# Performance work log

Measured on AMD Instinct MI355X. Metric: run time of the kernel, lower is better.

Reference implementation:

```python
import jax, jax.numpy as jnp
import numpy as np

MU, LMBD = 1000.0, 5000.0
C1, C2 = 0.5, 0.5
SPACING = 1.0
EPS = 1e-8

# Cyclic minor indices: the 2x2 minor of entry (m,i) of a 3x3 matrix uses rows
# (m+1, m+2) mod 3 and cols (i+1, i+2) mod 3; det of that minor IS the signed
# cofactor (so minorSigns3d == ones, matching the original module's contract).
_r = (np.arange(3)[:, None, None, None] + 1 + np.arange(2)[None, None, :, None]) % 3
_c = (np.arange(3)[None, :, None, None] + 1 + np.arange(2)[None, None, None, :]) % 3
ROW_IDX = np.broadcast_to(_r, (3, 3, 2, 2))  # (m,i,p,q) -> row index into 3x3
COL_IDX = np.broadcast_to(_c, (3, 3, 2, 2))  # (m,i,p,q) -> col index into 3x3


def _cof2(M):
    # signed cofactor matrix of 2x2 matrices; M: (..., 2, 2)
    a, b = M[..., 0, 0], M[..., 0, 1]
    c, d = M[..., 1, 0], M[..., 1, 1]
    return jnp.stack([jnp.stack([d, -c], -1), jnp.stack([-b, a], -1)], -2)


def _div_pk1_neohook(gradU, hessU, mu, lmbd):
    # gradU: (b,i,j,k,3,3)  [d2=component, d1=spatial deriv]
    # hessU: (b,i,j,k,3,3,3) [d2, d1, d3]
    F = gradU + jnp.eye(3, dtype=gradU.dtype)
    idxF = F[..., ROW_IDX, COL_IDX]                                   # (...,3,3,2,2)
    cofF = idxF[..., 0, 0] * idxF[..., 1, 1] - idxF[..., 0, 1] * idxF[..., 1, 0]  # (...,3,3)
    idxHess = hessU[..., ROW_IDX, COL_IDX, :]                          # (...,3,3,2,2,3)
    # d/dx_j det(minor(F)[m,i]) = cof2(minor) : d(minor)/dx_j
    gradCofF = jnp.einsum('...mipq,...mipqj->...mij', _cof2(idxF), idxHess)
    F0, cofF0 = F[..., :, 0], cofF[..., :, 0]
    J = jnp.einsum('...m,...m->...', F0, cofF0) + EPS                  # det(F), col-0 expansion
    invJ = 1.0 / J
    gradJ = jnp.einsum('...m,...mj->...j', cofF0, hessU[..., :, 0, :]) \
          + jnp.einsum('...mj,...m->...j', gradCofF[..., :, 0, :], F0)
    divInvF_T = -jnp.einsum('...,...j,...mj->...m', invJ * invJ, gradJ, cofF) \
              + invJ[..., None] * jnp.einsum('...mjj->...m', gradCofF)
    divF = jnp.einsum('...mjj->...m', hessU)
    divPK1 = mu * (divF - divInvF_T)
    divPK1 = divPK1 + 0.5 * lmbd * (J * J - 1.0)[..., None] * divInvF_T
    divPK1 = divPK1 + lmbd * jnp.einsum('...ij,...j->...i', cofF, gradJ)
    return divPK1


def _phy_loss(pred):
    # pred: (b,i,j,k,3); central differences interior, one-sided at edges
    gradU = jnp.stack(jnp.gradient(pred, axis=(1, 2, 3)), axis=-1) / SPACING   # (b,i,j,k,3,3)
    hessU = jnp.stack(jnp.gradient(gradU, axis=(1, 2, 3)), axis=-1) / SPACING  # (b,i,j,k,3,3,3)
    r = _div_pk1_neohook(gradU, hessU, MU, LMBD)
    r = jnp.where(jnp.isnan(r), 0.0, r)  # r[r != r] = 0
    return jnp.mean(jnp.linalg.norm(r, axis=-1))


def setup_inputs() -> dict:
    key = jax.random.key(0)
    k1, k2 = jax.random.split(key)
    shape = (4, 64, 64, 64, 3)
    prediction = 0.01 * jax.random.normal(k1, shape, dtype=jnp.float32)
    target = 0.01 * jax.random.normal(k2, shape, dtype=jnp.float32)
    return {"prediction": prediction, "target": target}


def reference(prediction, target):
    mse_loss = jnp.mean((prediction - target) ** 2)
    phy_loss = _phy_loss(prediction)
    return C1 * mse_loss + C2 * phy_loss
```

## Files before the change

kernel.cpp:

```cpp
#include <hip/hip_runtime.h>
#include <math.h>

#define ND 64
#define NPTS (4 * ND * ND * ND)
#define SXG (ND * ND * 3)
#define SYG (ND * 3)
#define XSEG 4

struct f3 { float v[3]; };

__device__ __forceinline__ f3 comb2(float a, const f3& X, float s, const f3& Y) {
    f3 r;
#pragma unroll
    for (int c = 0; c < 3; c++) r.v[c] = a * X.v[c] + s * Y.v[c];
    return r;
}
__device__ __forceinline__ f3 comb3(float a, const f3& X, float s, const f3& Y, float u, const f3& Z) {
    f3 r;
#pragma unroll
    for (int c = 0; c < 3; c++) r.v[c] = a * X.v[c] + s * Y.v[c] + u * Z.v[c];
    return r;
}

__device__ __forceinline__ float phys_norm(const float F[3][3], const float H[3][6]) {
    constexpr int SYM[3][3] = {{0, 3, 4}, {3, 1, 5}, {4, 5, 2}};

    float cof[3][3];
#pragma unroll
    for (int i = 0; i < 3; i++) {
        const int i1 = (i + 1) % 3, i2 = (i + 2) % 3;
#pragma unroll
        for (int j = 0; j < 3; j++) {
            const int j1 = (j + 1) % 3, j2 = (j + 2) % 3;
            cof[i][j] = F[i1][j1] * F[i2][j2] - F[i1][j2] * F[i2][j1];
        }
    }

    float gc0[3][3], trg[3];
#pragma unroll
    for (int m = 0; m < 3; m++) {
        const int m1 = (m + 1) % 3, m2 = (m + 2) % 3;
        trg[m] = 0.0f;
#pragma unroll
        for (int i = 0; i < 3; i++) {
            const int i1 = (i + 1) % 3, i2 = (i + 2) % 3;
#pragma unroll
            for (int j = 0; j < 3; j++) {
                if (i == 0 || i == j) {
                    const float g = F[m2][i2] * H[m1][SYM[i1][j]] + F[m1][i1] * H[m2][SYM[i2][j]]
                                  - F[m2][i1] * H[m1][SYM[i2][j]] - F[m1][i2] * H[m2][SYM[i1][j]];
                    if (i == 0) gc0[m][j] = g;
                    if (i == j) trg[m] += g;
                }
            }
        }
    }

    const float J = F[0][0] * cof[0][0] + F[1][0] * cof[1][0] + F[2][0] * cof[2][0] + 1e-8f;
    const float invJ = 1.0f / J;

    float gJ[3];
#pragma unroll
    for (int j = 0; j < 3; j++) {
        gJ[j] = cof[0][0] * H[0][SYM[0][j]] + cof[1][0] * H[1][SYM[0][j]] + cof[2][0] * H[2][SYM[0][j]]
              + gc0[0][j] * F[0][0] + gc0[1][j] * F[1][0] + gc0[2][j] * F[2][0];
    }

    const float MU = 1000.0f, LMBD = 5000.0f;
    const float halfL = 0.5f * LMBD * (J * J - 1.0f);
    float r[3];
#pragma unroll
    for (int m = 0; m < 3; m++) {
        const float s1 = gJ[0] * cof[m][0] + gJ[1] * cof[m][1] + gJ[2] * cof[m][2];
        const float divInv = -invJ * invJ * s1 + invJ * trg[m];
        const float divF = H[m][0] + H[m][1] + H[m][2];
        float v = MU * (divF - divInv) + halfL * divInv + LMBD * s1;
        r[m] = (v != v) ? 0.0f : v;
    }
    return sqrtf(r[0] * r[0] + r[1] * r[1] + r[2] * r[2]);
}

__device__ __forceinline__ void comp_row(
        float vC, float vXP, float vXM, float vYP, float vYM,
        float vXP2, float vXM2, float vYP2, float vYM2,
        float vPP, float vPM, float vMP, float vMM,
        int ip1, int im1, int ip2, int im2,
        bool l0, bool l1, bool l62, bool l63,
        float G[3], float Hr[6]) {
    const float d1r = __shfl(vC, ip1, 64), u1r = __shfl(vC, im1, 64);
    const float d2r = __shfl(vC, ip2, 64), u2r = __shfl(vC, im2, 64);
    const float d1 = l63 ? 2.f * vC - u1r : d1r;
    const float u1 = l0  ? 2.f * vC - d1r : u1r;
    const float d2 = l63 ? 4.f * vC - 4.f * u1r + u2r : (l62 ? 2.f * d1 - vC : d2r);
    const float u2 = l0  ? 4.f * vC - 4.f * d1r + d2r : (l1 ? 2.f * u1 - vC : u2r);

    const float g0 = 0.5f * (vXP - vXM);
    const float g1 = 0.5f * (vYP - vYM);
    G[0] = g0; G[1] = g1; G[2] = 0.5f * (d1 - u1);

    const float g0d = __shfl(g0, ip1, 64), g0u = __shfl(g0, im1, 64);
    const float g1d = __shfl(g1, ip1, 64), g1u = __shfl(g1, im1, 64);

    Hr[0] = 0.25f * (vXP2 + vXM2) - 0.5f * vC;
    Hr[1] = 0.25f * (vYP2 + vYM2) - 0.5f * vC;
    Hr[2] = 0.25f * (d2 + u2) - 0.5f * vC;
    Hr[3] = 0.25f * ((vPP - vMP) - (vPM - vMM));
    Hr[4] = 0.5f * ((l63 ? 2.f * g0 - g0u : g0d) - (l0 ? 2.f * g0 - g0d : g0u));
    Hr[5] = 0.5f * ((l63 ? 2.f * g1 - g1u : g1d) - (l0 ? 2.f * g1 - g1d : g1u));
}

__global__ __launch_bounds__(512) void phys_loss_kernel(
        const float* __restrict__ pred,
        const float* __restrict__ targ,
        float* __restrict__ out) {
    const int t = threadIdx.x;
    const int lane = t & 63;
    const int wid = t >> 6;
    const int w = blockIdx.x * 8 + wid;
    const int y = w & 63;
    const int xseg = (w >> 6) & 15;
    const int b = w >> 10;
    const int z = lane;
    const int X0 = xseg * XSEG;

    const float* __restrict__ pb = pred + (size_t)b * (ND * SXG);
    const int yc1p = min(y + 1, 63), yc1m = max(y - 1, 0);
    const int yc2p = min(y + 2, 63), yc2m = max(y - 2, 0);

#define LDP(gx, gy) (*(const f3*)(pb + (size_t)((gx) * SXG + (gy) * SYG + z * 3)))

    auto fixy1 = [&](const f3& ypl, const f3& yml, const f3& cg, f3& ypc, f3& ymc) {
        if (y == 0)       { ypc = ypl; ymc = comb2(2.f, cg, -1.f, ypl); }
        else if (y == 63) { ymc = yml; ypc = comb2(2.f, cg, -1.f, yml); }
        else              { ypc = ypl; ymc = yml; }
    };
    auto fixy2 = [&](const f3& yp2l, const f3& ym2l, const f3& c0,
                     const f3& yp1, const f3& ym1, f3& o_p, f3& o_m) {
        if (y == 0)       { o_p = yp2l; o_m = comb3(4.f, c0, -4.f, yp1, 1.f, yp2l); }
        else if (y == 1)  { o_p = yp2l; o_m = comb2(2.f, ym1, -1.f, c0); }
        else if (y == 62) { o_m = ym2l; o_p = comb2(2.f, yp1, -1.f, c0); }
        else if (y == 63) { o_m = ym2l; o_p = comb3(4.f, c0, -4.f, ym1, 1.f, ym2l); }
        else              { o_p = yp2l; o_m = ym2l; }
    };

    f3 cc[5], cyp[3], cym[3], yp2, ym2;
    if (X0 == 0) {
        cc[2] = LDP(0, y); cc[3] = LDP(1, y); cc[4] = LDP(2, y);
        cc[1] = comb2(2.f, cc[2], -1.f, cc[3]);
        cc[0] = comb3(4.f, cc[2], -4.f, cc[3], 1.f, cc[4]);
        { f3 a = LDP(0, yc1p), bq = LDP(0, yc1m); fixy1(a, bq, cc[2], cyp[1], cym[1]); }
        { f3 a = LDP(1, yc1p), bq = LDP(1, yc1m); fixy1(a, bq, cc[3], cyp[2], cym[2]); }
        cyp[0] = comb2(2.f, cyp[1], -1.f, cyp[2]);
        cym[0] = comb2(2.f, cym[1], -1.f, cym[2]);
    } else {
#pragma unroll
        for (int k = 0; k < 5; k++) cc[k] = LDP(X0 - 2 + k, y);
#pragma unroll
        for (int k = 0; k < 3; k++) {
            f3 a = LDP(X0 - 1 + k, yc1p), bq = LDP(X0 - 1 + k, yc1m);
            fixy1(a, bq, cc[k + 1], cyp[k], cym[k]);
        }
    }
    { f3 a = LDP(X0, yc2p), bq = LDP(X0, yc2m);
      fixy2(a, bq, cc[2], cyp[1], cym[1], yp2, ym2); }

    const bool l0 = (z == 0), l1 = (z == 1), l62 = (z == 62), l63 = (z == 63);
    const int ip1 = (lane + 1) & 63, im1 = (lane + 63) & 63;
    const int ip2 = (lane + 2) & 63, im2 = (lane + 62) & 63;

    float accn = 0.f, accs = 0.f;

#pragma unroll
    for (int i = 0; i < XSEG; i++) {
        const int x0 = X0 + i;

        f3 cin, ypin, ymin, yp2in, ym2in;
        if (i < XSEG - 1) {
            const int gxc = min(x0 + 3, 63);
            const int gx1 = min(x0 + 2, 63);
            cin  = LDP(gxc, y);
            ypin = LDP(gx1, yc1p);  ymin = LDP(gx1, yc1m);
            yp2in = LDP(x0 + 1, yc2p);  ym2in = LDP(x0 + 1, yc2m);
        }
        const f3 T = *(const f3*)(targ + (size_t)b * (ND * SXG)
                                  + (size_t)(x0 * SXG + y * SYG + z * 3));

        float F[3][3], H[3][6], G[3];
        comp_row(cc[2].v[0], cc[3].v[0], cc[1].v[0], cyp[1].v[0], cym[1].v[0],
                 cc[4].v[0], cc[0].v[0], yp2.v[0], ym2.v[0],
                 cyp[2].v[0], cym[2].v[0], cyp[0].v[0], cym[0].v[0],
                 ip1, im1, ip2, im2, l0, l1, l62, l63, G, H[0]);
        F[0][0] = G[0] + 1.f; F[0][1] = G[1]; F[0][2] = G[2];
        comp_row(cc[2].v[1], cc[3].v[1], cc[1].v[1], cyp[1].v[1], cym[1].v[1],
                 cc[4].v[1], cc[0].v[1], yp2.v[1], ym2.v[1],
                 cyp[2].v[1], cym[2].v[1], cyp[0].v[1], cym[0].v[1],
                 ip1, im1, ip2, im2, l0, l1, l62, l63, G, H[1]);
        F[1][0] = G[0]; F[1][1] = G[1] + 1.f; F[1][2] = G[2];
        comp_row(cc[2].v[2], cc[3].v[2], cc[1].v[2], cyp[1].v[2], cym[1].v[2],
                 cc[4].v[2], cc[0].v[2], yp2.v[2], ym2.v[2],
                 cyp[2].v[2], cym[2].v[2], cyp[0].v[2], cym[0].v[2],
                 ip1, im1, ip2, im2, l0, l1, l62, l63, G, H[2]);
        F[2][0] = G[0]; F[2][1] = G[1]; F[2][2] = G[2] + 1.f;

        accn += phys_norm(F, H);

        const float dx = cc[2].v[0] - T.v[0];
        const float dy = cc[2].v[1] - T.v[1];
        const float dz = cc[2].v[2] - T.v[2];
        accs += dx * dx + dy * dy + dz * dz;

        if (i < XSEG - 1) {
            cc[0] = cc[1]; cc[1] = cc[2]; cc[2] = cc[3]; cc[3] = cc[4];
            cyp[0] = cyp[1]; cyp[1] = cyp[2];
            cym[0] = cym[1]; cym[1] = cym[2];
            const int nx0 = x0 + 1;
            if (nx0 + 2 <= 63)      cc[4] = cin;
            else if (nx0 + 2 == 64) cc[4] = comb2(2.f, cc[3], -1.f, cc[2]);
            else                    cc[4] = comb3(4.f, cc[2], -4.f, cc[1], 1.f, cc[0]);
            if (nx0 + 1 <= 63) {
                fixy1(ypin, ymin, cc[3], cyp[2], cym[2]);
            } else {
                cyp[2] = comb2(2.f, cyp[1], -1.f, cyp[0]);
                cym[2] = comb2(2.f, cym[1], -1.f, cym[0]);
            }
            fixy2(yp2in, ym2in, cc[2], cyp[1], cym[1], yp2, ym2);
        }
    }
#undef LDP

    const float invN = 1.0f / (float)NPTS;
    float val = 0.5f * accs * (invN * (1.0f / 3.0f)) + 0.5f * accn * invN;

#pragma unroll
    for (int off = 32; off > 0; off >>= 1) val += __shfl_down(val, off, 64);

    __shared__ float wsum[8];
    if (lane == 0) wsum[wid] = val;
    __syncthreads();
    if (t == 0) {
        float acc = 0.0f;
#pragma unroll
        for (int wq = 0; wq < 8; wq++) acc += wsum[wq];
        atomicAdd(out, acc);
    }
}

extern "C" void kernel_launch(void* const* d_in, const int* in_sizes, int n_in,
                              void* d_out, int out_size, void* d_ws, size_t ws_size,
                              hipStream_t stream) {
    const float* pred = (const float*)d_in[0];
    const float* targ = (const float*)d_in[1];
    float* out = (float*)d_out;

    hipMemsetAsync(out, 0, sizeof(float), stream);

    const int blocks = (4 * 64 * (64 / XSEG)) / 8;
    phys_loss_kernel<<<blocks, 512, 0, stream>>>(pred, targ, out);
}
```

Before: 33.90 us.

## Lengthen x-segments and replace z-boundary branches with per-lane stencil coefficients

Doubles the number of x-planes each wavefront marches through (XSEG 4 to 8), which halves the grid to 256 blocks and cuts redundant halo loads at segment starts. The z-direction one-sided boundary selects are replaced by per-lane coefficient sets that are precomputed once, so every lane runs the same FMA expression. The x-loop is only partially unrolled (unroll 2) to keep register pressure down. The risk is lower occupancy, with fewer blocks than ideal for the CU count, plus loop overhead from partial unrolling.

Result: faster. 29.34 us (median of 2 runs) (-13.4%).

```diff
diff --git a/kernel.cpp b/kernel.cpp
--- a/kernel.cpp
+++ b/kernel.cpp
@@ -5,7 +5,7 @@
 #define NPTS (4 * ND * ND * ND)
 #define SXG (ND * ND * 3)
 #define SYG (ND * 3)
-#define XSEG 4
+#define XSEG 8
 
 struct f3 { float v[3]; };
 
@@ -80,33 +80,26 @@
     return sqrtf(r[0] * r[0] + r[1] * r[1] + r[2] * r[2]);
 }
 
+struct ZC { float a1, a2, a3, b1, b2, b3, b4, b5, e1, e2, e3; };
+
 __device__ __forceinline__ void comp_row(
-        float vC, float vXP, float vXM, float vYP, float vYM,
-        float vXP2, float vXM2, float vYP2, float vYM2,
-        float vPP, float vPM, float vMP, float vMM,
-        int ip1, int im1, int ip2, int im2,
-        bool l0, bool l1, bool l62, bool l63,
+        float vC, float Sx, float Sy, float sx2, float sy2, float dga,
+        int ip1, int im1, int ip2, int im2, const ZC& q,
         float G[3], float Hr[6]) {
     const float d1r = __shfl(vC, ip1, 64), u1r = __shfl(vC, im1, 64);
     const float d2r = __shfl(vC, ip2, 64), u2r = __shfl(vC, im2, 64);
-    const float d1 = l63 ? 2.f * vC - u1r : d1r;
-    const float u1 = l0  ? 2.f * vC - d1r : u1r;
-    const float d2 = l63 ? 4.f * vC - 4.f * u1r + u2r : (l62 ? 2.f * d1 - vC : d2r);
-    const float u2 = l0  ? 4.f * vC - 4.f * d1r + d2r : (l1 ? 2.f * u1 - vC : u2r);
-
-    const float g0 = 0.5f * (vXP - vXM);
-    const float g1 = 0.5f * (vYP - vYM);
-    G[0] = g0; G[1] = g1; G[2] = 0.5f * (d1 - u1);
-
-    const float g0d = __shfl(g0, ip1, 64), g0u = __shfl(g0, im1, 64);
-    const float g1d = __shfl(g1, ip1, 64), g1u = __shfl(g1, im1, 64);
-
-    Hr[0] = 0.25f * (vXP2 + vXM2) - 0.5f * vC;
-    Hr[1] = 0.25f * (vYP2 + vYM2) - 0.5f * vC;
-    Hr[2] = 0.25f * (d2 + u2) - 0.5f * vC;
-    Hr[3] = 0.25f * ((vPP - vMP) - (vPM - vMM));
-    Hr[4] = 0.5f * ((l63 ? 2.f * g0 - g0u : g0d) - (l0 ? 2.f * g0 - g0d : g0u));
-    Hr[5] = 0.5f * ((l63 ? 2.f * g1 - g1u : g1d) - (l0 ? 2.f * g1 - g1d : g1u));
+    const float Dx = __shfl(Sx, ip1, 64), Ux = __shfl(Sx, im1, 64);
+    const float Dy = __shfl(Sy, ip1, 64), Uy = __shfl(Sy, im1, 64);
+
+    G[0] = 0.5f * Sx;
+    G[1] = 0.5f * Sy;
+    G[2] = q.a1 * d1r + q.a2 * u1r + q.a3 * vC;
+    Hr[0] = 0.25f * sx2 - 0.5f * vC;
+    Hr[1] = 0.25f * sy2 - 0.5f * vC;
+    Hr[2] = q.b1 * d1r + q.b2 * u1r + q.b3 * d2r + q.b4 * u2r + q.b5 * vC;
+    Hr[3] = 0.25f * dga;
+    Hr[4] = q.e1 * Dx + q.e2 * Ux + q.e3 * Sx;
+    Hr[5] = q.e1 * Dy + q.e2 * Uy + q.e3 * Sy;
 }
 
 __global__ __launch_bounds__(512) void phys_loss_kernel(
@@ -118,12 +111,13 @@
     const int wid = t >> 6;
     const int w = blockIdx.x * 8 + wid;
     const int y = w & 63;
-    const int xseg = (w >> 6) & 15;
-    const int b = w >> 10;
+    const int xseg = (w >> 6) & 7;
+    const int b = w >> 9;
     const int z = lane;
     const int X0 = xseg * XSEG;
 
     const float* __restrict__ pb = pred + (size_t)b * (ND * SXG);
+    const float* __restrict__ tb = targ + (size_t)b * (ND * SXG);
     const int yc1p = min(y + 1, 63), yc1m = max(y - 1, 0);
     const int yc2p = min(y + 2, 63), yc2m = max(y - 2, 0);
 
@@ -164,13 +158,18 @@
     { f3 a = LDP(X0, yc2p), bq = LDP(X0, yc2m);
       fixy2(a, bq, cc[2], cyp[1], cym[1], yp2, ym2); }
 
-    const bool l0 = (z == 0), l1 = (z == 1), l62 = (z == 62), l63 = (z == 63);
+    ZC q = {0.5f, -0.5f, 0.f,  0.f, 0.f, 0.25f, 0.25f, -0.5f,  0.25f, -0.25f, 0.f};
+    if (z == 0)  { q = {1.f, 0.f, -1.f,  -1.f, 0.f, 0.5f, 0.f, 0.5f,   0.5f, 0.f, -0.5f}; }
+    if (z == 1)  { q.b1 = 0.f; q.b2 = 0.5f; q.b3 = 0.25f; q.b4 = 0.f; q.b5 = -0.75f; }
+    if (z == 62) { q.b1 = 0.5f; q.b2 = 0.f; q.b3 = 0.f; q.b4 = 0.25f; q.b5 = -0.75f; }
+    if (z == 63) { q = {0.f, -1.f, 1.f,  0.f, -1.f, 0.f, 0.5f, 0.5f,  0.f, -0.5f, 0.5f}; }
+
     const int ip1 = (lane + 1) & 63, im1 = (lane + 63) & 63;
     const int ip2 = (lane + 2) & 63, im2 = (lane + 62) & 63;
 
     float accn = 0.f, accs = 0.f;
 
-#pragma unroll
+#pragma unroll 2
     for (int i = 0; i < XSEG; i++) {
         const int x0 = X0 + i;
 
@@ -182,25 +181,22 @@
             ypin = LDP(gx1, yc1p);  ymin = LDP(gx1, yc1m);
             yp2in = LDP(x0 + 1, yc2p);  ym2in = LDP(x0 + 1, yc2m);
         }
-        const f3 T = *(const f3*)(targ + (size_t)b * (ND * SXG)
-                                  + (size_t)(x0 * SXG + y * SYG + z * 3));
+        const f3 T = *(const f3*)(tb + (size_t)(x0 * SXG + y * SYG + z * 3));
 
         float F[3][3], H[3][6], G[3];
-        comp_row(cc[2].v[0], cc[3].v[0], cc[1].v[0], cyp[1].v[0], cym[1].v[0],
-                 cc[4].v[0], cc[0].v[0], yp2.v[0], ym2.v[0],
-                 cyp[2].v[0], cym[2].v[0], cyp[0].v[0], cym[0].v[0],
-                 ip1, im1, ip2, im2, l0, l1, l62, l63, G, H[0]);
-        F[0][0] = G[0] + 1.f; F[0][1] = G[1]; F[0][2] = G[2];
-        comp_row(cc[2].v[1], cc[3].v[1], cc[1].v[1], cyp[1].v[1], cym[1].v[1],
-                 cc[4].v[1], cc[0].v[1], yp2.v[1], ym2.v[1],
-                 cyp[2].v[1], cym[2].v[1], cyp[0].v[1], cym[0].v[1],
-                 ip1, im1, ip2, im2, l0, l1, l62, l63, G, H[1]);
-        F[1][0] = G[0]; F[1][1] = G[1] + 1.f; F[1][2] = G[2];
-        comp_row(cc[2].v[2], cc[3].v[2], cc[1].v[2], cyp[1].v[2], cym[1].v[2],
-                 cc[4].v[2], cc[0].v[2], yp2.v[2], ym2.v[2],
-                 cyp[2].v[2], cym[2].v[2], cyp[0].v[2], cym[0].v[2],
-                 ip1, im1, ip2, im2, l0, l1, l62, l63, G, H[2]);
-        F[2][0] = G[0]; F[2][1] = G[1]; F[2][2] = G[2] + 1.f;
+#pragma unroll
+        for (int c = 0; c < 3; c++) {
+            const float Sx  = cc[3].v[c] - cc[1].v[c];
+            const float Sy  = cyp[1].v[c] - cym[1].v[c];
+            const float sx2 = cc[4].v[c] + cc[0].v[c];
+            const float sy2 = yp2.v[c] + ym2.v[c];
+            const float dga = (cyp[2].v[c] - cyp[0].v[c]) - (cym[2].v[c] - cym[0].v[c]);
+            comp_row(cc[2].v[c], Sx, Sy, sx2, sy2, dga,
+                     ip1, im1, ip2, im2, q, G, H[c]);
+            F[c][0] = G[0] + ((c == 0) ? 1.f : 0.f);
+            F[c][1] = G[1] + ((c == 1) ? 1.f : 0.f);
+            F[c][2] = G[2] + ((c == 2) ? 1.f : 0.f);
+        }
 
         accn += phys_norm(F, H);
 
@@ -254,6 +250,6 @@
 
     hipMemsetAsync(out, 0, sizeof(float), stream);
 
-    const int blocks = (4 * 64 * (64 / XSEG)) / 8;
+    const int blocks = 256;
     phys_loss_kernel<<<blocks, 512, 0, stream>>>(pred, targ, out);
 }
```
